# Optimization experiments

Measured on AMD Instinct MI355X. Metric: run time of the kernel, lower is better.

The kernel has to match this reference:

```python
import jax, jax.numpy as jnp
import numpy as np

HIDDEN = 2048
N_HEADS = 16
Q_DIM = N_HEADS * 128  # 2048
INTER = 10944
EPS = 1e-6
B, S = 2, 2048


def rms_norm(x, w, eps):
    var = jnp.mean(jnp.square(x), axis=-1, keepdims=True)
    return x * jax.lax.rsqrt(var + eps) * w


def setup_inputs() -> dict:
    key = jax.random.key(0)
    ks = jax.random.split(key, 8)
    x = jax.random.normal(ks[0], (B, S, HIDDEN), dtype=jnp.float32)
    positions = jnp.broadcast_to(jnp.arange(S, dtype=jnp.int32), (B, S))
    sc = 0.02
    return {
        "x": x,
        "positions": positions,
        "in_w": jnp.ones((HIDDEN,), dtype=jnp.float32),
        "post_w": jnp.ones((HIDDEN,), dtype=jnp.float32),
        "Wq": jax.random.normal(ks[1], (Q_DIM, HIDDEN), dtype=jnp.float32) * sc,
        "Wo": jax.random.normal(ks[2], (HIDDEN, Q_DIM), dtype=jnp.float32) * sc,
        "Wg": jax.random.normal(ks[3], (INTER, HIDDEN), dtype=jnp.float32) * sc,
        "Wu": jax.random.normal(ks[4], (INTER, HIDDEN), dtype=jnp.float32) * sc,
        "Wd": jax.random.normal(ks[5], (HIDDEN, INTER), dtype=jnp.float32) * sc,
    }


def reference(x, positions, in_w, post_w, Wq, Wo, Wg, Wu, Wd):
    b, s, h = x.shape
    xf = x.reshape(-1, h)                       # [T, H]
    h_norm = rms_norm(xf, in_w, EPS)            # RMSNorm (input_layernorm)
    q = jnp.einsum('th,qh->tq', h_norm, Wq)     # q_proj
    hidden = xf + jnp.einsum('tq,hq->th', q, Wo)  # o_proj + residual
    h_post = rms_norm(hidden, post_w, EPS)      # post_attention_layernorm
    gate = jax.nn.silu(jnp.einsum('th,ih->ti', h_post, Wg))
    up = jnp.einsum('th,ih->ti', h_post, Wu)
    mlp = jnp.einsum('ti,hi->th', gate * up, Wd)  # down_proj
    return (hidden + mlp).reshape(b, s, h)
```

## Files before the change

### kernel.cpp

```cpp
#include <hip/hip_runtime.h>
#include <hip/hip_bf16.h>
#include <stdint.h>


typedef __bf16 bf16;
typedef bf16 bf16x8 __attribute__((ext_vector_type(8)));
typedef bf16 bf16x4 __attribute__((ext_vector_type(4)));
typedef float f32x4 __attribute__((ext_vector_type(4)));

#define HID     2048
#define TOK     4096
#define INTER   10944
#define INTER_P 11008

__device__ __forceinline__ void gload_lds16(const bf16* g, bf16* l) {
    __builtin_amdgcn_global_load_lds(
        (const __attribute__((address_space(1))) void*)g,
        (__attribute__((address_space(3))) void*)l, 16, 0, 0);
}

#define SBAR()      asm volatile("s_barrier" ::: "memory")
#define WAIT_BAR(n) asm volatile("s_waitcnt vmcnt(" #n ")\n\ts_barrier" ::: "memory")
#define FMA16(d, a, b) d = __builtin_amdgcn_mfma_f32_16x16x32_bf16(a, b, d, 0, 0, 0)

__global__ __launch_bounds__(256) void conv_pad(const float* __restrict__ src,
                                                bf16* __restrict__ dst,
                                                int n_src, int n_dst) {
    int i = (blockIdx.x * 256 + threadIdx.x) * 4;
    if (i >= n_dst) return;
    float4 v = make_float4(0.f, 0.f, 0.f, 0.f);
    if (i < n_src) v = *(const float4*)(src + i);
    bf16x4 o;
    o[0] = (bf16)v.x; o[1] = (bf16)v.y; o[2] = (bf16)v.z; o[3] = (bf16)v.w;
    *(bf16x4*)(dst + i) = o;
}

__global__ __launch_bounds__(256) void conv_wd(const float* __restrict__ src,
                                               bf16* __restrict__ dst) {
    int i = (blockIdx.x * 256 + threadIdx.x) * 4;
    if (i >= HID * INTER_P) return;
    int row = i / INTER_P;
    int col = i - row * INTER_P;
    float4 v = make_float4(0.f, 0.f, 0.f, 0.f);
    if (col < INTER)
        v = *(const float4*)(src + (size_t)row * INTER + col);
    bf16x4 o;
    o[0] = (bf16)v.x; o[1] = (bf16)v.y; o[2] = (bf16)v.z; o[3] = (bf16)v.w;
    *(bf16x4*)(dst + i) = o;
}

__global__ __launch_bounds__(256) void rmsnorm_k(const float* __restrict__ x,
                                                 const float* __restrict__ w,
                                                 bf16* __restrict__ out) {
    const int row = blockIdx.x;
    const int tid = threadIdx.x;
    const float* xr = x + (size_t)row * HID + tid * 8;
    float4 v0 = *(const float4*)(xr);
    float4 v1 = *(const float4*)(xr + 4);
    float s = v0.x * v0.x + v0.y * v0.y + v0.z * v0.z + v0.w * v0.w +
              v1.x * v1.x + v1.y * v1.y + v1.z * v1.z + v1.w * v1.w;
    #pragma unroll
    for (int o = 32; o > 0; o >>= 1) s += __shfl_down(s, o);
    __shared__ float red[4];
    if ((tid & 63) == 0) red[tid >> 6] = s;
    __syncthreads();
    float tot = red[0] + red[1] + red[2] + red[3];
    float scale = rsqrtf(tot * (1.0f / (float)HID) + 1e-6f);
    float4 w0 = *(const float4*)(w + tid * 8);
    float4 w1 = *(const float4*)(w + tid * 8 + 4);
    bf16x8 o8;
    o8[0] = (bf16)(v0.x * scale * w0.x);
    o8[1] = (bf16)(v0.y * scale * w0.y);
    o8[2] = (bf16)(v0.z * scale * w0.z);
    o8[3] = (bf16)(v0.w * scale * w0.w);
    o8[4] = (bf16)(v1.x * scale * w1.x);
    o8[5] = (bf16)(v1.y * scale * w1.y);
    o8[6] = (bf16)(v1.z * scale * w1.z);
    o8[7] = (bf16)(v1.w * scale * w1.w);
    *(bf16x8*)(out + (size_t)row * HID + tid * 8) = o8;
}

#define ABUF2 16384
#define WBUF2 8192
#define BUFE2 24576

#define STGA(b, kk, i) gload_lds16(sA[i] + (kk), &lds[(b) * BUFE2 + (i) * 4096 + ldst])
#define STGW(b, kk, j) gload_lds16(sW[j] + (kk), &lds[(b) * BUFE2 + ABUF2 + (j) * 4096 + ldst])

template <int EPI>
__global__ __launch_bounds__(512, 2) void gemm_p2(const bf16* __restrict__ A,
                                                  const bf16* __restrict__ W,
                                                  const float* __restrict__ res,
                                                  void* __restrict__ out,
                                                  int N, int K) {
    extern __shared__ bf16 lds[];
    const int tid = threadIdx.x;
    const int rowBase = blockIdx.x * 256;
    const int colBase = blockIdx.y * 128;
    const int wave = tid >> 6, lane = tid & 63;
    const int wm = wave >> 1, wn = wave & 1;
    const int fr = lane & 15, kq = lane >> 4;

    const int slr = tid >> 3;
    const int sc  = (tid & 7) ^ (slr & 7);
    const bf16* sA[4];
    #pragma unroll
    for (int i = 0; i < 4; ++i)
        sA[i] = A + (size_t)(rowBase + i * 64 + slr) * K + sc * 8;
    const bf16* sW[2];
    #pragma unroll
    for (int j = 0; j < 2; ++j)
        sW[j] = W + (size_t)(colBase + j * 64 + slr) * K + sc * 8;
    const int ldst = tid * 8;

    int aof[2][2][2], wof[2][2][2];
    #pragma unroll
    for (int q = 0; q < 2; ++q)
      #pragma unroll
      for (int ii = 0; ii < 2; ++ii) {
        const int ra = wm * 64 + q * 32 + ii * 16 + fr;
        const int rw = wn * 64 + q * 32 + ii * 16 + fr;
        #pragma unroll
        for (int ks = 0; ks < 2; ++ks) {
            aof[q][ii][ks] = ra * 64 + (((ks * 4 + kq) ^ (ra & 7)) * 8);
            wof[q][ii][ks] = ABUF2 + rw * 64 + (((ks * 4 + kq) ^ (rw & 7)) * 8);
        }
      }

    f32x4 acc[4][4] = {};
    bf16x8 af[2][2], w0[2][2], w1[2][2];
    const int NT = K >> 6;

    STGA(0, 0, 0); STGA(0, 0, 1); STGA(0, 0, 2); STGA(0, 0, 3);
    STGW(0, 0, 0); STGW(0, 0, 1);
    STGA(1, 64, 0); STGA(1, 64, 1); STGA(1, 64, 2); STGA(1, 64, 3);
    STGW(1, 64, 0); STGW(1, 64, 1);
    WAIT_BAR(6);

    int buf = 0, sbuf = 2;
    for (int t = 0; t < NT; ++t) {
        const int bb = buf * BUFE2;
        const bool st = (t + 2) < NT;
        const int kk = (t + 2) << 6;
        if (st) { STGA(sbuf, kk, 0); STGA(sbuf, kk, 1); }
        #pragma unroll
        for (int ii = 0; ii < 2; ++ii)
          #pragma unroll
          for (int ks = 0; ks < 2; ++ks) {
            af[ii][ks] = *(const bf16x8*)&lds[bb + aof[0][ii][ks]];
            w0[ii][ks] = *(const bf16x8*)&lds[bb + wof[0][ii][ks]];
          }
        SBAR();
        __builtin_amdgcn_s_setprio(1);
        #pragma unroll
        for (int ks = 0; ks < 2; ++ks)
          #pragma unroll
          for (int ii = 0; ii < 2; ++ii)
            #pragma unroll
            for (int jj = 0; jj < 2; ++jj)
                FMA16(acc[ii][jj], af[ii][ks], w0[jj][ks]);
        __builtin_amdgcn_s_setprio(0);
        SBAR();
        if (st) { STGA(sbuf, kk, 2); STGA(sbuf, kk, 3); }
        #pragma unroll
        for (int jj = 0; jj < 2; ++jj)
          #pragma unroll
          for (int ks = 0; ks < 2; ++ks)
            w1[jj][ks] = *(const bf16x8*)&lds[bb + wof[1][jj][ks]];
        SBAR();
        __builtin_amdgcn_s_setprio(1);
        #pragma unroll
        for (int ks = 0; ks < 2; ++ks)
          #pragma unroll
          for (int ii = 0; ii < 2; ++ii)
            #pragma unroll
            for (int jj = 0; jj < 2; ++jj)
                FMA16(acc[ii][2 + jj], af[ii][ks], w1[jj][ks]);
        __builtin_amdgcn_s_setprio(0);
        SBAR();
        if (st) STGW(sbuf, kk, 0);
        #pragma unroll
        for (int ii = 0; ii < 2; ++ii)
          #pragma unroll
          for (int ks = 0; ks < 2; ++ks)
            af[ii][ks] = *(const bf16x8*)&lds[bb + aof[1][ii][ks]];
        SBAR();
        __builtin_amdgcn_s_setprio(1);
        #pragma unroll
        for (int ks = 0; ks < 2; ++ks)
          #pragma unroll
          for (int ii = 0; ii < 2; ++ii)
            #pragma unroll
            for (int jj = 0; jj < 2; ++jj)
                FMA16(acc[2 + ii][2 + jj], af[ii][ks], w1[jj][ks]);
        __builtin_amdgcn_s_setprio(0);
        SBAR();
        if (st) STGW(sbuf, kk, 1);
        SBAR();
        __builtin_amdgcn_s_setprio(1);
        #pragma unroll
        for (int ks = 0; ks < 2; ++ks)
          #pragma unroll
          for (int ii = 0; ii < 2; ++ii)
            #pragma unroll
            for (int jj = 0; jj < 2; ++jj)
                FMA16(acc[2 + ii][jj], af[ii][ks], w0[jj][ks]);
        __builtin_amdgcn_s_setprio(0);
        if (st) WAIT_BAR(6); else WAIT_BAR(0);
        buf  = (buf  == 2) ? 0 : buf + 1;
        sbuf = (sbuf == 2) ? 0 : sbuf + 1;
    }
    const int rq = lane >> 4, cn = lane & 15;
    #pragma unroll
    for (int mi = 0; mi < 4; ++mi)
      #pragma unroll
      for (int nj = 0; nj < 4; ++nj) {
        const int col = colBase + wn * 64 + nj * 16 + cn;
        #pragma unroll
        for (int r = 0; r < 4; ++r) {
            const int row = rowBase + wm * 64 + mi * 16 + rq * 4 + r;
            const size_t idx = (size_t)row * N + col;
            const float v = acc[mi][nj][r];
            if (EPI == 0) ((bf16*)out)[idx] = (bf16)v;
            else          ((float*)out)[idx] = res[idx] + v;
        }
      }
}

#define ABUF3 8192
#define GBUF3 4096
#define BUFE3 16384

__global__ __launch_bounds__(512, 2) void gemm_gup(const bf16* __restrict__ A,
                                                   const bf16* __restrict__ Wg,
                                                   const bf16* __restrict__ Wu,
                                                   bf16* __restrict__ out,
                                                   int N, int K) {
    extern __shared__ bf16 lds[];
    const int tid = threadIdx.x;
    const int rowBase = blockIdx.x * 256;
    const int colBase = blockIdx.y * 128;
    const int wave = tid >> 6, lane = tid & 63;
    const int wm = wave >> 1, wn = wave & 1;
    const int fr = lane & 15, kq = lane >> 4;

    const int slr = tid >> 2;
    const int sc  = (tid & 3) ^ ((slr >> 1) & 3);
    const bf16* sA0 = A  + (size_t)(rowBase +       slr) * K + sc * 8;
    const bf16* sA1 = A  + (size_t)(rowBase + 128 + slr) * K + sc * 8;
    const bf16* sG  = Wg + (size_t)(colBase +       slr) * K + sc * 8;
    const bf16* sU  = Wu + (size_t)(colBase +       slr) * K + sc * 8;
    const int ldst = tid * 8;

    int aof[4], gof[2][2];
    #pragma unroll
    for (int mi = 0; mi < 4; ++mi) {
        const int r = wm * 64 + mi * 16 + fr;
        aof[mi] = r * 32 + ((kq ^ ((r >> 1) & 3)) * 8);
    }
    #pragma unroll
    for (int q = 0; q < 2; ++q)
      #pragma unroll
      for (int jj = 0; jj < 2; ++jj) {
        const int r = wn * 64 + q * 32 + jj * 16 + fr;
        gof[q][jj] = ABUF3 + r * 32 + ((kq ^ ((r >> 1) & 3)) * 8);
      }

    f32x4 ag[4][4] = {}, au[4][4] = {};
    bf16x8 af[4], gq[2], uq[2];
    const int NT = K >> 5;

    #pragma unroll
    for (int b = 0; b < 3; ++b) {
        gload_lds16(sA0 + b * 32, &lds[b * BUFE3 + ldst]);
        gload_lds16(sA1 + b * 32, &lds[b * BUFE3 + 4096 + ldst]);
        gload_lds16(sG  + b * 32, &lds[b * BUFE3 + ABUF3 + ldst]);
        gload_lds16(sU  + b * 32, &lds[b * BUFE3 + ABUF3 + GBUF3 + ldst]);
    }
    WAIT_BAR(8);

    int buf = 0, sbuf = 3;
    for (int t = 0; t < NT; ++t) {
        const int bb = buf * BUFE3;
        const bool st = (t + 3) < NT;
        const int kk = (t + 3) << 5;
        if (st) {
            gload_lds16(sA0 + kk, &lds[sbuf * BUFE3 + ldst]);
            gload_lds16(sA1 + kk, &lds[sbuf * BUFE3 + 4096 + ldst]);
        }
        #pragma unroll
        for (int mi = 0; mi < 4; ++mi)
            af[mi] = *(const bf16x8*)&lds[bb + aof[mi]];
        #pragma unroll
        for (int jj = 0; jj < 2; ++jj) {
            gq[jj] = *(const bf16x8*)&lds[bb + gof[0][jj]];
            uq[jj] = *(const bf16x8*)&lds[bb + gof[0][jj] + GBUF3];
        }
        SBAR();
        __builtin_amdgcn_s_setprio(1);
        #pragma unroll
        for (int mi = 0; mi < 4; ++mi)
          #pragma unroll
          for (int jj = 0; jj < 2; ++jj) {
            FMA16(ag[mi][jj], af[mi], gq[jj]);
            FMA16(au[mi][jj], af[mi], uq[jj]);
          }
        __builtin_amdgcn_s_setprio(0);
        SBAR();
        if (st) {
            gload_lds16(sG + kk, &lds[sbuf * BUFE3 + ABUF3 + ldst]);
            gload_lds16(sU + kk, &lds[sbuf * BUFE3 + ABUF3 + GBUF3 + ldst]);
        }
        #pragma unroll
        for (int jj = 0; jj < 2; ++jj) {
            gq[jj] = *(const bf16x8*)&lds[bb + gof[1][jj]];
            uq[jj] = *(const bf16x8*)&lds[bb + gof[1][jj] + GBUF3];
        }
        SBAR();
        __builtin_amdgcn_s_setprio(1);
        #pragma unroll
        for (int mi = 0; mi < 4; ++mi)
          #pragma unroll
          for (int jj = 0; jj < 2; ++jj) {
            FMA16(ag[mi][2 + jj], af[mi], gq[jj]);
            FMA16(au[mi][2 + jj], af[mi], uq[jj]);
          }
        __builtin_amdgcn_s_setprio(0);
        if (st)                WAIT_BAR(8);
        else if ((t + 2) < NT) WAIT_BAR(4);
        else                   WAIT_BAR(0);
        buf  = (buf + 1) & 3;
        sbuf = (sbuf + 1) & 3;
    }
    const int rq = lane >> 4, cn = lane & 15;
    #pragma unroll
    for (int mi = 0; mi < 4; ++mi)
      #pragma unroll
      for (int nj = 0; nj < 4; ++nj) {
        const int col = colBase + wn * 64 + nj * 16 + cn;
        #pragma unroll
        for (int r = 0; r < 4; ++r) {
            const int row = rowBase + wm * 64 + mi * 16 + rq * 4 + r;
            const float g = ag[mi][nj][r];
            const float u = au[mi][nj][r];
            const float sg = g / (1.0f + __expf(-g));
            out[(size_t)row * N + col] = (bf16)(sg * u);
        }
      }
}

extern "C" void kernel_launch(void* const* d_in, const int* in_sizes, int n_in,
                              void* d_out, int out_size, void* d_ws, size_t ws_size,
                              hipStream_t stream) {
    const float* x      = (const float*)d_in[0];
    const float* in_w   = (const float*)d_in[2];
    const float* post_w = (const float*)d_in[3];
    const float* Wq     = (const float*)d_in[4];
    const float* Wo     = (const float*)d_in[5];
    const float* Wg     = (const float*)d_in[6];
    const float* Wu     = (const float*)d_in[7];
    const float* Wd     = (const float*)d_in[8];

    hipFuncSetAttribute(reinterpret_cast<const void*>(&gemm_p2<0>),
                        hipFuncAttributeMaxDynamicSharedMemorySize, 3 * BUFE2 * 2);
    hipFuncSetAttribute(reinterpret_cast<const void*>(&gemm_p2<1>),
                        hipFuncAttributeMaxDynamicSharedMemorySize, 3 * BUFE2 * 2);
    hipFuncSetAttribute(reinterpret_cast<const void*>(&gemm_gup),
                        hipFuncAttributeMaxDynamicSharedMemorySize, 4 * BUFE3 * 2);

    char* ws = (char*)d_ws;
    bf16*  X    = (bf16*)(ws + 0);
    bf16*  Yq   = (bf16*)(ws + 16777216);
    float* hid  = (float*)(ws + 33554432);
    bf16*  gu   = (bf16*)(ws + 67108864);
    bf16*  w0   = (bf16*)(ws + 157286400);
    bf16*  w1   = (bf16*)(ws + 202375168);
    bf16*  wsm  = (bf16*)(ws + 247463936);

    const int nGU  = INTER_P * HID;
    const int nGUs = INTER * HID;
    const int nSq  = HID * HID;

    conv_pad<<<nGU / 4 / 256, 256, 0, stream>>>(Wg, w0, nGUs, nGU);
    conv_pad<<<nGU / 4 / 256, 256, 0, stream>>>(Wu, w1, nGUs, nGU);
    conv_pad<<<nSq / 4 / 256, 256, 0, stream>>>(Wq, wsm, nSq, nSq);

    rmsnorm_k<<<TOK, 256, 0, stream>>>(x, in_w, X);
    gemm_p2<0><<<dim3(TOK / 256, HID / 128), 512, 3 * BUFE2 * 2, stream>>>(
        X, wsm, nullptr, Yq, HID, HID);
    conv_pad<<<nSq / 4 / 256, 256, 0, stream>>>(Wo, wsm, nSq, nSq);
    gemm_p2<1><<<dim3(TOK / 256, HID / 128), 512, 3 * BUFE2 * 2, stream>>>(
        Yq, wsm, x, hid, HID, HID);
    rmsnorm_k<<<TOK, 256, 0, stream>>>(hid, post_w, X);
    gemm_gup<<<dim3(TOK / 256, INTER_P / 128), 512, 4 * BUFE3 * 2, stream>>>(
        X, w0, w1, gu, INTER_P, HID);
    conv_wd<<<nGU / 4 / 256, 256, 0, stream>>>(Wd, w0);
    gemm_p2<1><<<dim3(TOK / 256, HID / 128), 512, 3 * BUFE2 * 2, stream>>>(
        gu, w0, hid, (float*)d_out, HID, INTER_P);
}
```

Baseline: 967.2 us.

## Software-pipeline LDS fragment loads across iterations in both GEMM kernels

Restructures the main loops of the projection GEMM and the fused gate/up GEMM so the first fragments for the next k-tile are read from LDS during the current tile's final MFMA phase. Each phase now reads the operands for the following phase, and the vmcnt wait moves to mid-iteration ahead of the barrier. sched_barrier markers keep the compiler from reordering loads across the MFMA blocks. The aim is to hide LDS read latency behind matrix math, at the cost of more live vector registers and a subtler correctness argument about barriers and buffer reuse.

```diff
diff --git a/kernel.cpp b/kernel.cpp
--- a/kernel.cpp
+++ b/kernel.cpp
@@ -20,7 +20,9 @@
 }
 
 #define SBAR()      asm volatile("s_barrier" ::: "memory")
-#define WAIT_BAR(n) asm volatile("s_waitcnt vmcnt(" #n ")\n\ts_barrier" ::: "memory")
+#define VMCNT(n)    asm volatile("s_waitcnt vmcnt(" #n ")" ::: "memory")
+#define SCHED0()    __builtin_amdgcn_sched_barrier(0)
+#define PRIO(n)     __builtin_amdgcn_s_setprio(n)
 #define FMA16(d, a, b) d = __builtin_amdgcn_mfma_f32_16x16x32_bf16(a, b, d, 0, 0, 0)
 
 __global__ __launch_bounds__(256) void conv_pad(const float* __restrict__ src,
@@ -81,7 +83,6 @@
 }
 
 #define ABUF2 16384
-#define WBUF2 8192
 #define BUFE2 24576
 
 #define STGA(b, kk, i) gload_lds16(sA[i] + (kk), &lds[(b) * BUFE2 + (i) * 4096 + ldst])
@@ -128,87 +129,104 @@
       }
 
     f32x4 acc[4][4] = {};
-    bf16x8 af[2][2], w0[2][2], w1[2][2];
     const int NT = K >> 6;
 
     STGA(0, 0, 0); STGA(0, 0, 1); STGA(0, 0, 2); STGA(0, 0, 3);
     STGW(0, 0, 0); STGW(0, 0, 1);
     STGA(1, 64, 0); STGA(1, 64, 1); STGA(1, 64, 2); STGA(1, 64, 3);
     STGW(1, 64, 0); STGW(1, 64, 1);
-    WAIT_BAR(6);
+    VMCNT(6);
+    SBAR();
+    bf16x8 af0[2][2], w0[2][2];
+    #pragma unroll
+    for (int ii = 0; ii < 2; ++ii)
+      #pragma unroll
+      for (int ks = 0; ks < 2; ++ks) {
+        af0[ii][ks] = *(const bf16x8*)&lds[aof[0][ii][ks]];
+        w0[ii][ks]  = *(const bf16x8*)&lds[wof[0][ii][ks]];
+      }
 
     int buf = 0, sbuf = 2;
     for (int t = 0; t < NT; ++t) {
-        const int bb = buf * BUFE2;
+        const int bb  = buf * BUFE2;
+        const int nxt = (buf == 2) ? 0 : buf + 1;
+        const int bn  = nxt * BUFE2;
         const bool st = (t + 2) < NT;
-        const int kk = (t + 2) << 6;
+        const int kk  = (t + 2) << 6;
+        bf16x8 w1[2][2], af1[2][2], w0n[2][2], af0n[2][2];
         if (st) { STGA(sbuf, kk, 0); STGA(sbuf, kk, 1); }
         #pragma unroll
-        for (int ii = 0; ii < 2; ++ii)
-          #pragma unroll
-          for (int ks = 0; ks < 2; ++ks) {
-            af[ii][ks] = *(const bf16x8*)&lds[bb + aof[0][ii][ks]];
-            w0[ii][ks] = *(const bf16x8*)&lds[bb + wof[0][ii][ks]];
-          }
-        SBAR();
-        __builtin_amdgcn_s_setprio(1);
+        for (int jj = 0; jj < 2; ++jj)
+          #pragma unroll
+          for (int ks = 0; ks < 2; ++ks)
+            w1[jj][ks] = *(const bf16x8*)&lds[bb + wof[1][jj][ks]];
+        SBAR(); SCHED0();
+        PRIO(1);
         #pragma unroll
         for (int ks = 0; ks < 2; ++ks)
           #pragma unroll
           for (int ii = 0; ii < 2; ++ii)
             #pragma unroll
             for (int jj = 0; jj < 2; ++jj)
-                FMA16(acc[ii][jj], af[ii][ks], w0[jj][ks]);
-        __builtin_amdgcn_s_setprio(0);
-        SBAR();
+                FMA16(acc[ii][jj], af0[ii][ks], w0[jj][ks]);
+        PRIO(0); SCHED0(); SBAR();
         if (st) { STGA(sbuf, kk, 2); STGA(sbuf, kk, 3); }
         #pragma unroll
-        for (int jj = 0; jj < 2; ++jj)
+        for (int ii = 0; ii < 2; ++ii)
           #pragma unroll
           for (int ks = 0; ks < 2; ++ks)
-            w1[jj][ks] = *(const bf16x8*)&lds[bb + wof[1][jj][ks]];
-        SBAR();
-        __builtin_amdgcn_s_setprio(1);
+            af1[ii][ks] = *(const bf16x8*)&lds[bb + aof[1][ii][ks]];
+        if (st) VMCNT(4); else VMCNT(0);
+        SBAR(); SCHED0();
+        PRIO(1);
         #pragma unroll
         for (int ks = 0; ks < 2; ++ks)
           #pragma unroll
           for (int ii = 0; ii < 2; ++ii)
             #pragma unroll
             for (int jj = 0; jj < 2; ++jj)
-                FMA16(acc[ii][2 + jj], af[ii][ks], w1[jj][ks]);
-        __builtin_amdgcn_s_setprio(0);
-        SBAR();
+                FMA16(acc[ii][2 + jj], af0[ii][ks], w1[jj][ks]);
+        PRIO(0); SCHED0(); SBAR();
         if (st) STGW(sbuf, kk, 0);
         #pragma unroll
-        for (int ii = 0; ii < 2; ++ii)
+        for (int jj = 0; jj < 2; ++jj)
           #pragma unroll
           for (int ks = 0; ks < 2; ++ks)
-            af[ii][ks] = *(const bf16x8*)&lds[bb + aof[1][ii][ks]];
-        SBAR();
-        __builtin_amdgcn_s_setprio(1);
+            w0n[jj][ks] = *(const bf16x8*)&lds[bn + wof[0][jj][ks]];
+        SBAR(); SCHED0();
+        PRIO(1);
         #pragma unroll
         for (int ks = 0; ks < 2; ++ks)
           #pragma unroll
           for (int ii = 0; ii < 2; ++ii)
             #pragma unroll
             for (int jj = 0; jj < 2; ++jj)
-                FMA16(acc[2 + ii][2 + jj], af[ii][ks], w1[jj][ks]);
-        __builtin_amdgcn_s_setprio(0);
-        SBAR();
+                FMA16(acc[2 + ii][2 + jj], af1[ii][ks], w1[jj][ks]);
+        PRIO(0); SCHED0(); SBAR();
         if (st) STGW(sbuf, kk, 1);
-        SBAR();
-        __builtin_amdgcn_s_setprio(1);
+        #pragma unroll
+        for (int ii = 0; ii < 2; ++ii)
+          #pragma unroll
+          for (int ks = 0; ks < 2; ++ks)
+            af0n[ii][ks] = *(const bf16x8*)&lds[bn + aof[0][ii][ks]];
+        SBAR(); SCHED0();
+        PRIO(1);
         #pragma unroll
         for (int ks = 0; ks < 2; ++ks)
           #pragma unroll
           for (int ii = 0; ii < 2; ++ii)
             #pragma unroll
             for (int jj = 0; jj < 2; ++jj)
-                FMA16(acc[2 + ii][jj], af[ii][ks], w0[jj][ks]);
-        __builtin_amdgcn_s_setprio(0);
-        if (st) WAIT_BAR(6); else WAIT_BAR(0);
-        buf  = (buf  == 2) ? 0 : buf + 1;
-        sbuf = (sbuf == 2) ? 0 : sbuf + 1;
+                FMA16(acc[2 + ii][jj], af1[ii][ks], w0[jj][ks]);
+        PRIO(0); SCHED0(); SBAR();
+        #pragma unroll
+        for (int ii = 0; ii < 2; ++ii)
+          #pragma unroll
+          for (int ks = 0; ks < 2; ++ks) {
+            af0[ii][ks] = af0n[ii][ks];
+            w0[ii][ks]  = w0n[ii][ks];
+          }
+        buf = nxt; sbuf = (sbuf == 2) ? 0 : sbuf + 1;
     }
     const int rq = lane >> 4, cn = lane & 15;
     #pragma unroll
@@ -267,7 +285,6 @@
       }
 
     f32x4 ag[4][4] = {}, au[4][4] = {};
-    bf16x8 af[4], gq[2], uq[2];
     const int NT = K >> 5;
 
     #pragma unroll
@@ -277,14 +294,24 @@
         gload_lds16(sG  + b * 32, &lds[b * BUFE3 + ABUF3 + ldst]);
         gload_lds16(sU  + b * 32, &lds[b * BUFE3 + ABUF3 + GBUF3 + ldst]);
     }
-    WAIT_BAR(8);
+    VMCNT(8);
+    SBAR();
+    bf16x8 w0g[2], w0u[2];
+    #pragma unroll
+    for (int jj = 0; jj < 2; ++jj) {
+        w0g[jj] = *(const bf16x8*)&lds[gof[0][jj]];
+        w0u[jj] = *(const bf16x8*)&lds[gof[0][jj] + GBUF3];
+    }
 
     int buf = 0, sbuf = 3;
     for (int t = 0; t < NT; ++t) {
         const int bb = buf * BUFE3;
-        const bool st = (t + 3) < NT;
+        const int bn = ((buf + 1) & 3) * BUFE3;
+        const bool st3 = (t + 3) < NT;
+        const bool st2 = (t + 2) < NT;
         const int kk = (t + 3) << 5;
-        if (st) {
+        bf16x8 af[4], w1g[2], w1u[2], w0gn[2], w0un[2];
+        if (st3) {
             gload_lds16(sA0 + kk, &lds[sbuf * BUFE3 + ldst]);
             gload_lds16(sA1 + kk, &lds[sbuf * BUFE3 + 4096 + ldst]);
         }
@@ -293,43 +320,47 @@
             af[mi] = *(const bf16x8*)&lds[bb + aof[mi]];
         #pragma unroll
         for (int jj = 0; jj < 2; ++jj) {
-            gq[jj] = *(const bf16x8*)&lds[bb + gof[0][jj]];
-            uq[jj] = *(const bf16x8*)&lds[bb + gof[0][jj] + GBUF3];
-        }
-        SBAR();
-        __builtin_amdgcn_s_setprio(1);
+            w1g[jj] = *(const bf16x8*)&lds[bb + gof[1][jj]];
+            w1u[jj] = *(const bf16x8*)&lds[bb + gof[1][jj] + GBUF3];
+        }
+        if (st3)      VMCNT(6);
+        else if (st2) VMCNT(4);
+        else          VMCNT(0);
+        SBAR(); SCHED0();
+        PRIO(1);
         #pragma unroll
         for (int mi = 0; mi < 4; ++mi)
           #pragma unroll
           for (int jj = 0; jj < 2; ++jj) {
-            FMA16(ag[mi][jj], af[mi], gq[jj]);
-            FMA16(au[mi][jj], af[mi], uq[jj]);
+            FMA16(ag[mi][jj], af[mi], w0g[jj]);
+            FMA16(au[mi][jj], af[mi], w0u[jj]);
           }
-        __builtin_amdgcn_s_setprio(0);
-        SBAR();
-        if (st) {
+        PRIO(0); SCHED0(); SBAR();
+        if (st3) {
             gload_lds16(sG + kk, &lds[sbuf * BUFE3 + ABUF3 + ldst]);
             gload_lds16(sU + kk, &lds[sbuf * BUFE3 + ABUF3 + GBUF3 + ldst]);
         }
         #pragma unroll
         for (int jj = 0; jj < 2; ++jj) {
-            gq[jj] = *(const bf16x8*)&lds[bb + gof[1][jj]];
-            uq[jj] = *(const bf16x8*)&lds[bb + gof[1][jj] + GBUF3];
-        }
-        SBAR();
-        __builtin_amdgcn_s_setprio(1);
+            w0gn[jj] = *(const bf16x8*)&lds[bn + gof[0][jj]];
+            w0un[jj] = *(const bf16x8*)&lds[bn + gof[0][jj] + GBUF3];
+        }
+        SBAR(); SCHED0();
+        PRIO(1);
         #pragma unroll
         for (int mi = 0; mi < 4; ++mi)
           #pragma unroll
           for (int jj = 0; jj < 2; ++jj) {
-            FMA16(ag[mi][2 + jj], af[mi], gq[jj]);
-            FMA16(au[mi][2 + jj], af[mi], uq[jj]);
+            FMA16(ag[mi][2 + jj], af[mi], w1g[jj]);
+            FMA16(au[mi][2 + jj], af[mi], w1u[jj]);
           }
-        __builtin_amdgcn_s_setprio(0);
-        if (st)                WAIT_BAR(8);
-        else if ((t + 2) < NT) WAIT_BAR(4);
-        else                   WAIT_BAR(0);
-        buf  = (buf + 1) & 3;
+        PRIO(0); SCHED0(); SBAR();
+        #pragma unroll
+        for (int jj = 0; jj < 2; ++jj) {
+            w0g[jj] = w0gn[jj];
+            w0u[jj] = w0un[jj];
+        }
+        buf = (buf + 1) & 3;
         sbuf = (sbuf + 1) & 3;
     }
     const int rq = lane >> 4, cn = lane & 15;
```

Result: no change. 970.7 us (+0.4%).
